# Performance work log

Hardware: AMD Instinct MI355X
Metric: run time of the kernel (lower is better)

## Reference

```python
import jax, jax.numpy as jnp
import numpy as np

NT, NC, NM = 500_000, 100_000, 20_000   # transaction / client / merchant node counts
E = 500_000                              # edges per relation
IN, EMB, HID, OUT = 128, 64, 64, 2


def _lin_init(k, fan_in, fan_out):
    s = 1.0 / np.sqrt(fan_in)
    k1, k2 = jax.random.split(k)
    W = jax.random.uniform(k1, (fan_in, fan_out), jnp.float32, -s, s)
    b = jax.random.uniform(k2, (fan_out,), jnp.float32, -s, s)
    return W, b


def setup_inputs() -> dict:
    key = jax.random.key(0)
    ks = jax.random.split(key, 24)
    it = iter(range(24))
    d = {}
    d["features"] = jax.random.normal(ks[next(it)], (NT, IN), jnp.float32)
    d["emb_client"] = jax.random.normal(ks[next(it)], (NC, EMB), jnp.float32)
    d["emb_merchant"] = jax.random.normal(ks[next(it)], (NM, EMB), jnp.float32)
    for name, n_src, n_dst in [("c2t", NC, NT), ("m2t", NM, NT), ("t2c", NT, NC), ("t2m", NT, NM)]:
        d[f"src_{name}"] = jax.random.randint(ks[next(it)], (E,), 0, n_src)
        d[f"dst_{name}"] = jax.random.randint(ks[next(it)], (E,), 0, n_dst)
    # per-etype input size: in_size if src==transaction else embedding_size
    in0 = {"c2t": EMB, "m2t": EMB, "t2c": IN, "t2m": IN}
    for e in ["c2t", "m2t", "t2c", "t2m"]:
        d[f"W0_{e}"], d[f"b0_{e}"] = _lin_init(ks[next(it)], in0[e], HID)
        d[f"W1_{e}"], d[f"b1_{e}"] = _lin_init(ks[next(it)], HID, HID)
    d["Wf"], d["bf"] = _lin_init(ks[next(it)], HID, OUT)
    return d


def _seg_mean(msg, dst, n):
    # copy_u 'm' + mean reduce; zero in-degree dst nodes get 0 (DGL semantics)
    s = jax.ops.segment_sum(msg, dst, num_segments=n)
    cnt = jax.ops.segment_sum(jnp.ones((msg.shape[0], 1), msg.dtype), dst, num_segments=n)
    return s / jnp.maximum(cnt, 1.0)


def reference(features, emb_client, emb_merchant,
              src_c2t, dst_c2t, src_m2t, dst_m2t,
              src_t2c, dst_t2c, src_t2m, dst_t2m,
              W0_c2t, b0_c2t, W1_c2t, b1_c2t,
              W0_m2t, b0_m2t, W1_m2t, b1_m2t,
              W0_t2c, b0_t2c, W1_t2c, b1_t2c,
              W0_t2m, b0_t2m, W1_t2m, b1_t2m,
              Wf, bf):
    sizes = {"t": NT, "c": NC, "m": NM}
    edges = {"c2t": ("c", "t", src_c2t, dst_c2t),
             "m2t": ("m", "t", src_m2t, dst_m2t),
             "t2c": ("t", "c", src_t2c, dst_t2c),
             "t2m": ("t", "m", src_t2m, dst_t2m)}

    def rgcn_layer(h, W, b):
        acc = {}
        for e, (s, t, src, dst) in edges.items():
            wh = h[s] @ W[e] + b[e]                 # per-relation Linear on src nodes
            m = _seg_mean(wh[src], dst, sizes[t])   # gather + segment-mean
            acc[t] = acc.get(t, 0.0) + m            # cross-relation 'sum'
        return acc

    W0 = {"c2t": W0_c2t, "m2t": W0_m2t, "t2c": W0_t2c, "t2m": W0_t2m}
    b0 = {"c2t": b0_c2t, "m2t": b0_m2t, "t2c": b0_t2c, "t2m": b0_t2m}
    W1 = {"c2t": W1_c2t, "m2t": W1_m2t, "t2c": W1_t2c, "t2m": W1_t2m}
    b1 = {"c2t": b1_c2t, "m2t": b1_m2t, "t2c": b1_t2c, "t2m": b1_t2m}

    h = {"t": features, "c": emb_client, "m": emb_merchant}
    h = rgcn_layer(h, W0, b0)
    h = {k: jax.nn.leaky_relu(v) for k, v in h.items()}  # applied before layer i!=0
    h = rgcn_layer(h, W1, b1)
    return h["t"] @ Wf + bf                          # final Linear on target ntype
```

## Files before the change

### kernel.cpp

```cpp
#include <hip/hip_runtime.h>
#include <stdint.h>

#define NT 500000
#define NC 100000
#define NM 20000
#define NE 500000

__global__ __launch_bounds__(256) void weq_kernel(const float* __restrict__ W1c,
                                                  const float* __restrict__ b1c,
                                                  const float* __restrict__ W1m,
                                                  const float* __restrict__ b1m,
                                                  const float* __restrict__ Wf,
                                                  float* __restrict__ WeqC,
                                                  float* __restrict__ WeqM,
                                                  float* __restrict__ beq) {
    int t = threadIdx.x;
    if (t < 128) {
        int k = t >> 1, o = t & 1;
        float s = 0.0f;
        for (int j = 0; j < 64; j++) s += W1c[k * 64 + j] * Wf[j * 2 + o];
        WeqC[k * 2 + o] = s;
    } else {
        int k = (t - 128) >> 1, o = t & 1;
        float s = 0.0f;
        for (int j = 0; j < 64; j++) s += W1m[k * 64 + j] * Wf[j * 2 + o];
        WeqM[k * 2 + o] = s;
    }
    if (t < 4) {
        const float* b = (t < 2) ? b1c : b1m;
        int o = t & 1;
        float s = 0.0f;
        for (int j = 0; j < 64; j++) s += b[j] * Wf[j * 2 + o];
        beq[t] = s;
    }
}

__global__ __launch_bounds__(256) void chain4(const int* __restrict__ sTC,
                                              const int* __restrict__ dTC,
                                              const int* __restrict__ sTM,
                                              const int* __restrict__ dTM,
                                              const int* __restrict__ sCT,
                                              const int* __restrict__ dCT,
                                              const int* __restrict__ sMT,
                                              const int* __restrict__ dMT,
                                              int* __restrict__ headC,
                                              int* __restrict__ headM,
                                              int* __restrict__ headTC,
                                              int* __restrict__ headTM,
                                              int2* __restrict__ recC,
                                              int2* __restrict__ recM,
                                              int2* __restrict__ recTC,
                                              int2* __restrict__ recTM) {
    int id = blockIdx.x * 256 + threadIdx.x;
    int r = id / NE;
    if (r > 3) return;
    int e = id - r * NE;
    const int* src; const int* dst; int* head; int2* rec;
    if (r == 0)      { src = sTC; dst = dTC; head = headC;  rec = recC; }
    else if (r == 1) { src = sTM; dst = dTM; head = headM;  rec = recM; }
    else if (r == 2) { src = sCT; dst = dCT; head = headTC; rec = recTC; }
    else             { src = sMT; dst = dMT; head = headTM; rec = recTM; }
    int d = dst[e], s = src[e];
    int old = atomicExch(&head[d], e);
    rec[e] = make_int2(s, old);
}

__global__ __launch_bounds__(256) void agg_chain(const float* __restrict__ feat,
                                                 const int* __restrict__ head,
                                                 const int2* __restrict__ rec,
                                                 float* __restrict__ sum,
                                                 int* __restrict__ cntArr,
                                                 int base, int nNodes) {
    int gw = (blockIdx.x * 256 + threadIdx.x) >> 6;
    if (gw >= nNodes) return;
    int lane = threadIdx.x & 63;
    int node = base + gw;
    int e = head[node];
    float ax = 0.0f, ay = 0.0f;
    int cnt = 0;
    const float* fp = feat + lane * 2;
    while (e >= 0) {
        int2 rc = rec[e];
        const float2 v = *(const float2*)(fp + (size_t)rc.x * 128);
        ax += v.x; ay += v.y;
        cnt++;
        e = rc.y;
    }
    float2 o; o.x = ax; o.y = ay;
    *(float2*)(sum + (size_t)gw * 128 + lane * 2) = o;
    if (lane == 0) cntArr[node] = cnt;
}

__global__ __launch_bounds__(256) void h1proj(const float* __restrict__ sum,
                                              const int* __restrict__ cntB,
                                              const float* __restrict__ W0,
                                              const float* __restrict__ b0,
                                              const float* __restrict__ Weq,
                                              float* __restrict__ p, int n) {
    __shared__ float Ws[128 * 64];
    __shared__ float sums[32 * 128];
    int tid = threadIdx.x;
    int base = blockIdx.x * 32;
    {
        const float4* W4 = (const float4*)W0;
        float4* Ws4 = (float4*)Ws;
        for (int i = tid; i < 128 * 64 / 4; i += 256) Ws4[i] = W4[i];
    }
    {
        const float4* S4 = (const float4*)sum;
        float4* s4 = (float4*)sums;
        for (int i = tid; i < 32 * 128 / 4; i += 256) {
            int r = i >> 5;
            int row = base + r;
            float4 v;
            if (row < n) v = S4[(size_t)base * 32 + i];
            else { v.x = v.y = v.z = v.w = 0.0f; }
            s4[i] = v;
        }
    }
    __syncthreads();
    int col = tid & 63, wv = tid >> 6;
    float acc[8];
#pragma unroll
    for (int r = 0; r < 8; r++) acc[r] = 0.0f;
    const float* srow = &sums[wv * 8 * 128];
    for (int k = 0; k < 128; k += 4) {
        float w0_ = Ws[(k + 0) * 64 + col];
        float w1_ = Ws[(k + 1) * 64 + col];
        float w2_ = Ws[(k + 2) * 64 + col];
        float w3_ = Ws[(k + 3) * 64 + col];
#pragma unroll
        for (int r = 0; r < 8; r++) {
            const float4 s = *(const float4*)&srow[r * 128 + k];
            acc[r] += s.x * w0_ + s.y * w1_ + s.z * w2_ + s.w * w3_;
        }
    }
    float b0c = b0[col];
    float wq0 = Weq[col * 2 + 0], wq1 = Weq[col * 2 + 1];
#pragma unroll
    for (int r = 0; r < 8; r++) {
        int row = base + wv * 8 + r;
        int cn = 0;
        if (row < n) cn = cntB[row];
        float h = 0.0f;
        if (cn > 0) {
            float v = acc[r] / (float)cn + b0c;
            h = v > 0.0f ? v : 0.01f * v;
        }
        float p0 = h * wq0, p1 = h * wq1;
#pragma unroll
        for (int off = 32; off; off >>= 1) {
            p0 += __shfl_down(p0, off, 64);
            p1 += __shfl_down(p1, off, 64);
        }
        if (col == 0 && row < n) {
            p[(size_t)row * 2 + 0] = p0;
            p[(size_t)row * 2 + 1] = p1;
        }
    }
}

__global__ __launch_bounds__(256) void gather_final(const float* __restrict__ pC,
                                                    const int* __restrict__ headTC,
                                                    const int2* __restrict__ recTC,
                                                    const float* __restrict__ pM,
                                                    const int* __restrict__ headTM,
                                                    const int2* __restrict__ recTM,
                                                    const float* __restrict__ beq,
                                                    const float* __restrict__ bfv,
                                                    float* __restrict__ out) {
    int i = blockIdx.x * 256 + threadIdx.x;
    if (i >= NT) return;
    float r0 = bfv[0], r1 = bfv[1];
    {
        int e = headTC[i];
        if (e >= 0) {
            float a0 = 0.f, a1 = 0.f;
            int c = 0;
            while (e >= 0) {
                int2 rc = recTC[e];
                const float2 v = *(const float2*)(pC + (size_t)rc.x * 2);
                a0 += v.x; a1 += v.y;
                c++;
                e = rc.y;
            }
            float inv = 1.0f / (float)c;
            r0 += a0 * inv + beq[0];
            r1 += a1 * inv + beq[1];
        }
    }
    {
        int e = headTM[i];
        if (e >= 0) {
            float a0 = 0.f, a1 = 0.f;
            int c = 0;
            while (e >= 0) {
                int2 rc = recTM[e];
                const float2 v = *(const float2*)(pM + (size_t)rc.x * 2);
                a0 += v.x; a1 += v.y;
                c++;
                e = rc.y;
            }
            float inv = 1.0f / (float)c;
            r0 += a0 * inv + beq[2];
            r1 += a1 * inv + beq[3];
        }
    }
    float2 o; o.x = r0; o.y = r1;
    *(float2*)(out + (size_t)i * 2) = o;
}

extern "C" void kernel_launch(void* const* d_in, const int* in_sizes, int n_in,
                              void* d_out, int out_size, void* d_ws, size_t ws_size,
                              hipStream_t stream) {
    const float* feat = (const float*)d_in[0];
    const int* src_c2t = (const int*)d_in[3];
    const int* dst_c2t = (const int*)d_in[4];
    const int* src_m2t = (const int*)d_in[5];
    const int* dst_m2t = (const int*)d_in[6];
    const int* src_t2c = (const int*)d_in[7];
    const int* dst_t2c = (const int*)d_in[8];
    const int* src_t2m = (const int*)d_in[9];
    const int* dst_t2m = (const int*)d_in[10];
    const float* W1_c2t = (const float*)d_in[13];
    const float* b1_c2t = (const float*)d_in[14];
    const float* W1_m2t = (const float*)d_in[17];
    const float* b1_m2t = (const float*)d_in[18];
    const float* W0_t2c = (const float*)d_in[19];
    const float* b0_t2c = (const float*)d_in[20];
    const float* W0_t2m = (const float*)d_in[23];
    const float* b0_t2m = (const float*)d_in[24];
    const float* Wf  = (const float*)d_in[27];
    const float* bfv = (const float*)d_in[28];

    char* ws = (char*)d_ws;
    float* SUM     = (float*)(ws + 0);
    int*   headC   = (int*)(ws + 25600000);
    int*   headM   = (int*)(ws + 26000000);
    int*   headTC  = (int*)(ws + 26080000);
    int*   headTM  = (int*)(ws + 28080000);
    int2*  recC    = (int2*)(ws + 30080000);
    int2*  recM    = (int2*)(ws + 34080000);
    int2*  recTC   = (int2*)(ws + 38080000);
    int2*  recTM   = (int2*)(ws + 42080000);
    float* pC      = (float*)(ws + 46080000);
    float* pM      = (float*)(ws + 46880000);
    int*   cntC    = (int*)(ws + 47040000);
    int*   cntM    = (int*)(ws + 47440000);
    float* WeqC    = (float*)(ws + 47520000);
    float* WeqM    = (float*)(ws + 47520512);
    float* beq     = (float*)(ws + 47521024);

    hipMemsetAsync(headC, 0xFF, 4480000, stream);

    weq_kernel<<<1, 256, 0, stream>>>(W1_c2t, b1_c2t, W1_m2t, b1_m2t, Wf, WeqC, WeqM, beq);

    chain4<<<7813, 256, 0, stream>>>(src_t2c, dst_t2c, src_t2m, dst_t2m,
                                     src_c2t, dst_c2t, src_m2t, dst_m2t,
                                     headC, headM, headTC, headTM,
                                     recC, recM, recTC, recTM);

    agg_chain<<<12500, 256, 0, stream>>>(feat, headC, recC, SUM, cntC, 0, 50000);
    h1proj<<<1563, 256, 0, stream>>>(SUM, cntC, W0_t2c, b0_t2c, WeqC, pC, 50000);
    agg_chain<<<12500, 256, 0, stream>>>(feat, headC, recC, SUM, cntC, 50000, 50000);
    h1proj<<<1563, 256, 0, stream>>>(SUM, cntC + 50000, W0_t2c, b0_t2c, WeqC, pC + 100000, 50000);
    agg_chain<<<5000, 256, 0, stream>>>(feat, headM, recM, SUM, cntM, 0, 20000);
    h1proj<<<625, 256, 0, stream>>>(SUM, cntM, W0_t2m, b0_t2m, WeqM, pM, 20000);

    gather_final<<<1954, 256, 0, stream>>>(pC, headTC, recTC,
                                           pM, headTM, recTM,
                                           beq, bfv, (float*)d_out);
}
```

Measured before the change: 739.0 us.

## Fuse neighbor aggregation with layer-0 projection into one kernel with interleaved chains

Merges the per-node linked-list aggregation and the 128x64 projection into a single kernel covering both client and merchant nodes. Partial sums stay in shared memory instead of going through a global SUM buffer, and six launches become one. Each wave walks two node chains at once for more memory-level parallelism, and gather_final walks its two chains in one interleaved loop. The cost is reloading the 32KB weight tile into shared memory per 16-node block, which is twice as often per node as before.

```diff
diff --git a/kernel.cpp b/kernel.cpp
--- a/kernel.cpp
+++ b/kernel.cpp
@@ -5,6 +5,9 @@
 #define NC 100000
 #define NM 20000
 #define NE 500000
+
+#define CBLK 6250
+#define MBLK 1250
 
 __global__ __launch_bounds__(256) void weq_kernel(const float* __restrict__ W1c,
                                                   const float* __restrict__ b1c,
@@ -65,86 +68,87 @@
     rec[e] = make_int2(s, old);
 }
 
-__global__ __launch_bounds__(256) void agg_chain(const float* __restrict__ feat,
-                                                 const int* __restrict__ head,
-                                                 const int2* __restrict__ rec,
-                                                 float* __restrict__ sum,
-                                                 int* __restrict__ cntArr,
-                                                 int base, int nNodes) {
-    int gw = (blockIdx.x * 256 + threadIdx.x) >> 6;
-    if (gw >= nNodes) return;
-    int lane = threadIdx.x & 63;
-    int node = base + gw;
-    int e = head[node];
-    float ax = 0.0f, ay = 0.0f;
-    int cnt = 0;
-    const float* fp = feat + lane * 2;
-    while (e >= 0) {
-        int2 rc = rec[e];
-        const float2 v = *(const float2*)(fp + (size_t)rc.x * 128);
-        ax += v.x; ay += v.y;
-        cnt++;
-        e = rc.y;
-    }
-    float2 o; o.x = ax; o.y = ay;
-    *(float2*)(sum + (size_t)gw * 128 + lane * 2) = o;
-    if (lane == 0) cntArr[node] = cnt;
-}
-
-__global__ __launch_bounds__(256) void h1proj(const float* __restrict__ sum,
-                                              const int* __restrict__ cntB,
-                                              const float* __restrict__ W0,
-                                              const float* __restrict__ b0,
-                                              const float* __restrict__ Weq,
-                                              float* __restrict__ p, int n) {
+__global__ __launch_bounds__(256) void agg_proj(const float* __restrict__ feat,
+                                                const int* __restrict__ headC,
+                                                const int2* __restrict__ recC,
+                                                const int* __restrict__ headM,
+                                                const int2* __restrict__ recM,
+                                                const float* __restrict__ W0C,
+                                                const float* __restrict__ b0C,
+                                                const float* __restrict__ WqC,
+                                                const float* __restrict__ W0M,
+                                                const float* __restrict__ b0M,
+                                                const float* __restrict__ WqM,
+                                                float* __restrict__ pC,
+                                                float* __restrict__ pM) {
     __shared__ float Ws[128 * 64];
-    __shared__ float sums[32 * 128];
+    __shared__ float sst[4][4][128];
     int tid = threadIdx.x;
-    int base = blockIdx.x * 32;
+    bool isM = blockIdx.x >= CBLK;
+    const int* head; const int2* rec; const float* W0; const float* b0; const float* Wq;
+    float* p; int base;
+    if (!isM) { head = headC; rec = recC; W0 = W0C; b0 = b0C; Wq = WqC; p = pC;
+                base = blockIdx.x * 16; }
+    else      { head = headM; rec = recM; W0 = W0M; b0 = b0M; Wq = WqM; p = pM;
+                base = (blockIdx.x - CBLK) * 16; }
     {
         const float4* W4 = (const float4*)W0;
         float4* Ws4 = (float4*)Ws;
-        for (int i = tid; i < 128 * 64 / 4; i += 256) Ws4[i] = W4[i];
-    }
-    {
-        const float4* S4 = (const float4*)sum;
-        float4* s4 = (float4*)sums;
-        for (int i = tid; i < 32 * 128 / 4; i += 256) {
-            int r = i >> 5;
-            int row = base + r;
-            float4 v;
-            if (row < n) v = S4[(size_t)base * 32 + i];
-            else { v.x = v.y = v.z = v.w = 0.0f; }
-            s4[i] = v;
-        }
+        for (int i = tid; i < 2048; i += 256) Ws4[i] = W4[i];
+    }
+    int lane = tid & 63, wv = tid >> 6;
+    const float* fp = feat + lane * 2;
+    int cn[4];
+#pragma unroll
+    for (int pr = 0; pr < 2; pr++) {
+        int n0 = base + wv * 4 + pr * 2;
+        int e0 = head[n0];
+        int e1 = head[n0 + 1];
+        float ax0 = 0.f, ay0 = 0.f, ax1 = 0.f, ay1 = 0.f;
+        int c0 = 0, c1 = 0;
+        while (e0 >= 0 || e1 >= 0) {
+            if (e0 >= 0) {
+                int2 rc = rec[e0];
+                const float2 v = *(const float2*)(fp + (size_t)rc.x * 128);
+                ax0 += v.x; ay0 += v.y; c0++; e0 = rc.y;
+            }
+            if (e1 >= 0) {
+                int2 rc = rec[e1];
+                const float2 v = *(const float2*)(fp + (size_t)rc.x * 128);
+                ax1 += v.x; ay1 += v.y; c1++; e1 = rc.y;
+            }
+        }
+        *(float2*)&sst[wv][pr * 2 + 0][lane * 2] = make_float2(ax0, ay0);
+        *(float2*)&sst[wv][pr * 2 + 1][lane * 2] = make_float2(ax1, ay1);
+        cn[pr * 2 + 0] = c0;
+        cn[pr * 2 + 1] = c1;
     }
     __syncthreads();
-    int col = tid & 63, wv = tid >> 6;
-    float acc[8];
+    int col = lane;
+    float a0 = 0.f, a1 = 0.f, a2 = 0.f, a3 = 0.f;
+#pragma unroll 4
+    for (int k = 0; k < 128; k += 4) {
+        float w0 = Ws[(k + 0) * 64 + col];
+        float w1 = Ws[(k + 1) * 64 + col];
+        float w2 = Ws[(k + 2) * 64 + col];
+        float w3 = Ws[(k + 3) * 64 + col];
+        const float4 s0 = *(const float4*)&sst[wv][0][k];
+        const float4 s1 = *(const float4*)&sst[wv][1][k];
+        const float4 s2 = *(const float4*)&sst[wv][2][k];
+        const float4 s3 = *(const float4*)&sst[wv][3][k];
+        a0 += s0.x * w0 + s0.y * w1 + s0.z * w2 + s0.w * w3;
+        a1 += s1.x * w0 + s1.y * w1 + s1.z * w2 + s1.w * w3;
+        a2 += s2.x * w0 + s2.y * w1 + s2.z * w2 + s2.w * w3;
+        a3 += s3.x * w0 + s3.y * w1 + s3.z * w2 + s3.w * w3;
+    }
+    float b0c = b0[col];
+    float wq0 = Wq[col * 2 + 0], wq1 = Wq[col * 2 + 1];
+    float acc[4] = {a0, a1, a2, a3};
 #pragma unroll
-    for (int r = 0; r < 8; r++) acc[r] = 0.0f;
-    const float* srow = &sums[wv * 8 * 128];
-    for (int k = 0; k < 128; k += 4) {
-        float w0_ = Ws[(k + 0) * 64 + col];
-        float w1_ = Ws[(k + 1) * 64 + col];
-        float w2_ = Ws[(k + 2) * 64 + col];
-        float w3_ = Ws[(k + 3) * 64 + col];
-#pragma unroll
-        for (int r = 0; r < 8; r++) {
-            const float4 s = *(const float4*)&srow[r * 128 + k];
-            acc[r] += s.x * w0_ + s.y * w1_ + s.z * w2_ + s.w * w3_;
-        }
-    }
-    float b0c = b0[col];
-    float wq0 = Weq[col * 2 + 0], wq1 = Weq[col * 2 + 1];
-#pragma unroll
-    for (int r = 0; r < 8; r++) {
-        int row = base + wv * 8 + r;
-        int cn = 0;
-        if (row < n) cn = cntB[row];
+    for (int j = 0; j < 4; j++) {
         float h = 0.0f;
-        if (cn > 0) {
-            float v = acc[r] / (float)cn + b0c;
+        if (cn[j] > 0) {
+            float v = acc[j] / (float)cn[j] + b0c;
             h = v > 0.0f ? v : 0.01f * v;
         }
         float p0 = h * wq0, p1 = h * wq1;
@@ -153,9 +157,10 @@
             p0 += __shfl_down(p0, off, 64);
             p1 += __shfl_down(p1, off, 64);
         }
-        if (col == 0 && row < n) {
-            p[(size_t)row * 2 + 0] = p0;
-            p[(size_t)row * 2 + 1] = p1;
+        if (lane == 0) {
+            int node = base + wv * 4 + j;
+            p[(size_t)node * 2 + 0] = p0;
+            p[(size_t)node * 2 + 1] = p1;
         }
     }
 }
@@ -171,40 +176,32 @@
                                                     float* __restrict__ out) {
     int i = blockIdx.x * 256 + threadIdx.x;
     if (i >= NT) return;
+    int e0 = headTC[i];
+    int e1 = headTM[i];
+    float c0a = 0.f, c0b = 0.f, c1a = 0.f, c1b = 0.f;
+    int n0 = 0, n1 = 0;
+    while (e0 >= 0 || e1 >= 0) {
+        if (e0 >= 0) {
+            int2 rc = recTC[e0];
+            const float2 v = *(const float2*)(pC + (size_t)rc.x * 2);
+            c0a += v.x; c0b += v.y; n0++; e0 = rc.y;
+        }
+        if (e1 >= 0) {
+            int2 rc = recTM[e1];
+            const float2 v = *(const float2*)(pM + (size_t)rc.x * 2);
+            c1a += v.x; c1b += v.y; n1++; e1 = rc.y;
+        }
+    }
     float r0 = bfv[0], r1 = bfv[1];
-    {
-        int e = headTC[i];
-        if (e >= 0) {
-            float a0 = 0.f, a1 = 0.f;
-            int c = 0;
-            while (e >= 0) {
-                int2 rc = recTC[e];
-                const float2 v = *(const float2*)(pC + (size_t)rc.x * 2);
-                a0 += v.x; a1 += v.y;
-                c++;
-                e = rc.y;
-            }
-            float inv = 1.0f / (float)c;
-            r0 += a0 * inv + beq[0];
-            r1 += a1 * inv + beq[1];
-        }
-    }
-    {
-        int e = headTM[i];
-        if (e >= 0) {
-            float a0 = 0.f, a1 = 0.f;
-            int c = 0;
-            while (e >= 0) {
-                int2 rc = recTM[e];
-                const float2 v = *(const float2*)(pM + (size_t)rc.x * 2);
-                a0 += v.x; a1 += v.y;
-                c++;
-                e = rc.y;
-            }
-            float inv = 1.0f / (float)c;
-            r0 += a0 * inv + beq[2];
-            r1 += a1 * inv + beq[3];
-        }
+    if (n0 > 0) {
+        float inv = 1.0f / (float)n0;
+        r0 += c0a * inv + beq[0];
+        r1 += c0b * inv + beq[1];
+    }
+    if (n1 > 0) {
+        float inv = 1.0f / (float)n1;
+        r0 += c1a * inv + beq[2];
+        r1 += c1b * inv + beq[3];
     }
     float2 o; o.x = r0; o.y = r1;
     *(float2*)(out + (size_t)i * 2) = o;
@@ -234,22 +231,19 @@
     const float* bfv = (const float*)d_in[28];
 
     char* ws = (char*)d_ws;
-    float* SUM     = (float*)(ws + 0);
-    int*   headC   = (int*)(ws + 25600000);
-    int*   headM   = (int*)(ws + 26000000);
-    int*   headTC  = (int*)(ws + 26080000);
-    int*   headTM  = (int*)(ws + 28080000);
-    int2*  recC    = (int2*)(ws + 30080000);
-    int2*  recM    = (int2*)(ws + 34080000);
-    int2*  recTC   = (int2*)(ws + 38080000);
-    int2*  recTM   = (int2*)(ws + 42080000);
-    float* pC      = (float*)(ws + 46080000);
-    float* pM      = (float*)(ws + 46880000);
-    int*   cntC    = (int*)(ws + 47040000);
-    int*   cntM    = (int*)(ws + 47440000);
-    float* WeqC    = (float*)(ws + 47520000);
-    float* WeqM    = (float*)(ws + 47520512);
-    float* beq     = (float*)(ws + 47521024);
+    int*   headC   = (int*)(ws + 0);
+    int*   headM   = (int*)(ws + 400000);
+    int*   headTC  = (int*)(ws + 480000);
+    int*   headTM  = (int*)(ws + 2480000);
+    int2*  recC    = (int2*)(ws + 4480000);
+    int2*  recM    = (int2*)(ws + 8480000);
+    int2*  recTC   = (int2*)(ws + 12480000);
+    int2*  recTM   = (int2*)(ws + 16480000);
+    float* pC      = (float*)(ws + 20480000);
+    float* pM      = (float*)(ws + 21280000);
+    float* WeqC    = (float*)(ws + 21440000);
+    float* WeqM    = (float*)(ws + 21440512);
+    float* beq     = (float*)(ws + 21441024);
 
     hipMemsetAsync(headC, 0xFF, 4480000, stream);
 
@@ -260,12 +254,10 @@
                                      headC, headM, headTC, headTM,
                                      recC, recM, recTC, recTM);
 
-    agg_chain<<<12500, 256, 0, stream>>>(feat, headC, recC, SUM, cntC, 0, 50000);
-    h1proj<<<1563, 256, 0, stream>>>(SUM, cntC, W0_t2c, b0_t2c, WeqC, pC, 50000);
-    agg_chain<<<12500, 256, 0, stream>>>(feat, headC, recC, SUM, cntC, 50000, 50000);
-    h1proj<<<1563, 256, 0, stream>>>(SUM, cntC + 50000, W0_t2c, b0_t2c, WeqC, pC + 100000, 50000);
-    agg_chain<<<5000, 256, 0, stream>>>(feat, headM, recM, SUM, cntM, 0, 20000);
-    h1proj<<<625, 256, 0, stream>>>(SUM, cntM, W0_t2m, b0_t2m, WeqM, pM, 20000);
+    agg_proj<<<CBLK + MBLK, 256, 0, stream>>>(feat, headC, recC, headM, recM,
+                                              W0_t2c, b0_t2c, WeqC,
+                                              W0_t2m, b0_t2m, WeqM,
+                                              pC, pM);
 
     gather_final<<<1954, 256, 0, stream>>>(pC, headTC, recTC,
                                            pM, headTM, recTM,
```

After: 807.7 us. 1.09x slower.
